# Optimization experiments

Hardware: AMD Instinct MI355X
Metric: run time of the kernel (lower is better)

Reference implementation:

```python
import jax, jax.numpy as jnp
import numpy as np

INPUT_DIM = 1024
OUTPUT_DIM = 1024


def setup_inputs() -> dict:
    key = jax.random.key(0)
    k1, k2, k3, k4 = jax.random.split(key, 4)
    B, S, D = 4, 2048, INPUT_DIM
    src = jax.random.normal(k1, (B, S, D), dtype=jnp.float32)
    tgt = jax.random.normal(k2, (B, S, D), dtype=jnp.float32)
    # nn.Linear(input_dim*2, output_dim): weight [out, in], bias [out]
    bound = 1.0 / np.sqrt(2 * D)
    W = jax.random.uniform(k3, (OUTPUT_DIM, 2 * D), jnp.float32, -bound, bound)
    b = jax.random.uniform(k4, (OUTPUT_DIM,), jnp.float32, -bound, bound)
    return {"src": src, "tgt": tgt, "W": W, "b": b}


def reference(src, tgt, W, b):
    # weight = bmm(tgt, src^T): [B, S_tgt, S_src]
    weight = jnp.einsum("btd,bsd->bts", tgt, src)
    # NOTE: original uses Softmax(dim=1) -> normalizes over the tgt axis
    weight = jax.nn.softmax(weight, axis=1)
    # weighted sum over src positions: [B, S_tgt, D]
    weight_sum = jnp.einsum("bts,bsd->btd", weight, src)
    output = jnp.concatenate([weight_sum, tgt], axis=2)  # [B, S_tgt, 2D]
    output = output @ W.T + b  # [B, S_tgt, output_dim]
    return (output, weight)
```

## Files before the change

kernel.cpp:

```cpp
#include <hip/hip_runtime.h>
#include <stdint.h>


#define B_   4
#define S_   2048
#define D_   1024
#define OUTD 1024

typedef unsigned short ushort_t;
typedef _Float16 half8 __attribute__((ext_vector_type(8)));
typedef float    f32x4 __attribute__((ext_vector_type(4)));

__device__ __forceinline__ ushort_t f2h(float f) {
    union { _Float16 h; ushort_t u; } v;
    v.h = (_Float16)f;
    return v.u;
}
__device__ __forceinline__ float h2f(ushort_t u) {
    union { _Float16 h; ushort_t u; } v;
    v.u = u;
    return (float)v.h;
}

__device__ __forceinline__ void ld16(const ushort_t* g, ushort_t* l) {
    __builtin_amdgcn_global_load_lds(
        (const __attribute__((address_space(1))) void*)g,
        (__attribute__((address_space(3))) void*)l, 16, 0, 0);
}


__global__ void k_split(const float4* __restrict__ src, const float4* __restrict__ tgt,
                        ushort4* __restrict__ sh,
                        ushort4* __restrict__ th, ushort4* __restrict__ tl)
{
    const int64_t n4 = (int64_t)B_ * S_ * D_ / 4;
    for (int64_t i = (int64_t)blockIdx.x * blockDim.x + threadIdx.x; i < n4;
         i += (int64_t)gridDim.x * blockDim.x) {
        float4 s = src[i];
        sh[i] = (ushort4){f2h(s.x), f2h(s.y), f2h(s.z), f2h(s.w)};
        float4 tv = tgt[i];
        ushort4 ht = {f2h(tv.x), f2h(tv.y), f2h(tv.z), f2h(tv.w)};
        th[i] = ht;
        tl[i] = (ushort4){f2h(tv.x - h2f(ht.x)), f2h(tv.y - h2f(ht.y)),
                          f2h(tv.z - h2f(ht.z)), f2h(tv.w - h2f(ht.w))};
    }
}

__global__ void k_wconv(const float4* __restrict__ W, ushort4* __restrict__ wb)
{
    const int64_t n4 = (int64_t)OUTD * 2 * D_ / 4;
    for (int64_t i = (int64_t)blockIdx.x * blockDim.x + threadIdx.x; i < n4;
         i += (int64_t)gridDim.x * blockDim.x) {
        float4 w = W[i];
        wb[i] = (ushort4){f2h(w.x), f2h(w.y), f2h(w.z), f2h(w.w)};
    }
}

__launch_bounds__(512, 2)
__global__ void k_gemm_logits(const ushort_t* __restrict__ Ah, const ushort_t* __restrict__ Al,
                              const ushort_t* __restrict__ Bs,
                              float* __restrict__ C,
                              float* __restrict__ pm, float* __restrict__ ps)
{
    const int M = S_, N = S_, K = D_;
    int b = blockIdx.z;
    Ah += (int64_t)b * M * K;  Al += (int64_t)b * M * K;
    Bs += (int64_t)b * N * K;
    C  += (int64_t)b * M * N;

    __shared__ __align__(16) ushort_t lds[2 * 24576];
    __shared__ float red_m[4][256], red_s[4][256];

    int t    = threadIdx.x;
    int m0   = blockIdx.y * 256, n0 = blockIdx.x * 256;
    int wave = t >> 6, lane = t & 63;
    int wr   = (wave >> 1) * 64;
    int wc   = (wave & 1) * 128;
    int l15  = lane & 15, quad = lane >> 4;

    f32x4 acc[4][8];
#pragma unroll
    for (int i = 0; i < 4; i++)
#pragma unroll
        for (int j = 0; j < 8; j++) acc[i][j] = (f32x4){0.f, 0.f, 0.f, 0.f};

    int pr   = t >> 3;
    int slot = t & 7;
    int cg   = slot ^ (pr & 7);
    int srow = pr * 2 + (cg >> 2);
    int scol = (cg & 3) * 8;

    const ushort_t* gAh = Ah + (int64_t)(m0 + srow) * K + scol;
    const ushort_t* gAl = Al + (int64_t)(m0 + srow) * K + scol;
    const ushort_t* gB  = Bs + (int64_t)(n0 + srow) * K + scol;
    const int64_t rstep = (int64_t)128 * K;

    auto stage = [&](int bufi, int kofs) {
        ushort_t* Lb = lds + bufi * 24576 + t * 8;
        ld16(gAh + kofs,         Lb);
        ld16(gAh + rstep + kofs, Lb + 4096);
        ld16(gAl + kofs,         Lb + 8192);
        ld16(gAl + rstep + kofs, Lb + 12288);
        ld16(gB  + kofs,         Lb + 16384);
        ld16(gB  + rstep + kofs, Lb + 20480);
    };

    int aoff[4], boff[8];
#pragma unroll
    for (int i = 0; i < 4; i++) {
        int R = wr + i * 16 + l15;
        int p = R >> 1, c = ((R & 1) << 2) + quad;
        aoff[i] = p * 64 + ((c ^ (p & 7)) << 3);
    }
#pragma unroll
    for (int j = 0; j < 8; j++) {
        int R = wc + j * 16 + l15;
        int p = R >> 1, c = ((R & 1) << 2) + quad;
        boff[j] = p * 64 + ((c ^ (p & 7)) << 3);
    }

    stage(0, 0);
    int buf = 0;

    for (int kt = 0; kt < 32; ++kt) {
        asm volatile("s_waitcnt vmcnt(0)" ::: "memory");
        __builtin_amdgcn_s_barrier();
        asm volatile("" ::: "memory");
        __builtin_amdgcn_sched_barrier(0);

        if (kt < 31) stage(buf ^ 1, (kt + 1) * 32);

        const ushort_t* Lb = lds + buf * 24576;
        half8 ah[4], al[4], bf[4];
#pragma unroll
        for (int i = 0; i < 4; i++) {
            ah[i] = *(const half8*)(Lb + aoff[i]);
            al[i] = *(const half8*)(Lb + 8192 + aoff[i]);
        }
#pragma unroll
        for (int j = 0; j < 4; j++) bf[j] = *(const half8*)(Lb + 16384 + boff[j]);

        __builtin_amdgcn_s_setprio(1);
#pragma unroll
        for (int i = 0; i < 4; i++)
#pragma unroll
            for (int j = 0; j < 4; j++)
                acc[i][j] = __builtin_amdgcn_mfma_f32_16x16x32_f16(ah[i], bf[j], acc[i][j], 0, 0, 0);
#pragma unroll
        for (int i = 0; i < 4; i++)
#pragma unroll
            for (int j = 0; j < 4; j++)
                acc[i][j] = __builtin_amdgcn_mfma_f32_16x16x32_f16(al[i], bf[j], acc[i][j], 0, 0, 0);
        __builtin_amdgcn_s_setprio(0);

#pragma unroll
        for (int j = 0; j < 4; j++) bf[j] = *(const half8*)(Lb + 16384 + boff[4 + j]);

        __builtin_amdgcn_s_setprio(1);
#pragma unroll
        for (int i = 0; i < 4; i++)
#pragma unroll
            for (int j = 0; j < 4; j++)
                acc[i][4 + j] = __builtin_amdgcn_mfma_f32_16x16x32_f16(ah[i], bf[j], acc[i][4 + j], 0, 0, 0);
#pragma unroll
        for (int i = 0; i < 4; i++)
#pragma unroll
            for (int j = 0; j < 4; j++)
                acc[i][4 + j] = __builtin_amdgcn_mfma_f32_16x16x32_f16(al[i], bf[j], acc[i][4 + j], 0, 0, 0);
        __builtin_amdgcn_s_setprio(0);

        buf ^= 1;
    }

#pragma unroll
    for (int i = 0; i < 4; i++) {
        int row_base = m0 + wr + i * 16 + quad * 4;
#pragma unroll
        for (int j = 0; j < 8; j++) {
            int col = n0 + wc + j * 16 + l15;
#pragma unroll
            for (int r = 0; r < 4; r++)
                C[(int64_t)(row_base + r) * N + col] = acc[i][j][r];
        }
    }

    int wrow = wave >> 1;
#pragma unroll
    for (int j = 0; j < 8; j++) {
        float m = -3.0e38f;
#pragma unroll
        for (int i = 0; i < 4; i++)
#pragma unroll
            for (int r = 0; r < 4; r++) m = fmaxf(m, acc[i][j][r]);
        float s = 0.f;
#pragma unroll
        for (int i = 0; i < 4; i++)
#pragma unroll
            for (int r = 0; r < 4; r++) s += __expf(acc[i][j][r] - m);
#pragma unroll
        for (int d = 16; d <= 32; d <<= 1) {
            float m2 = __shfl_xor(m, d, 64);
            float s2 = __shfl_xor(s, d, 64);
            float nm = fmaxf(m, m2);
            s = s * __expf(m - nm) + s2 * __expf(m2 - nm);
            m = nm;
        }
        if (lane < 16) {
            red_m[wrow][wc + j * 16 + l15] = m;
            red_s[wrow][wc + j * 16 + l15] = s;
        }
    }
    __syncthreads();
    if (t < 256) {
        float m = red_m[0][t];
#pragma unroll
        for (int w = 1; w < 4; w++) m = fmaxf(m, red_m[w][t]);
        float s = 0.f;
#pragma unroll
        for (int w = 0; w < 4; w++) s += red_s[w][t] * __expf(red_m[w][t] - m);
        int idx = blockIdx.y * (B_ * S_) + b * S_ + n0 + t;
        pm[idx] = m;
        ps[idx] = s;
    }
}


__global__ void k_colstats2(const float* __restrict__ pm, const float* __restrict__ ps,
                            float* __restrict__ cmax, float* __restrict__ cinv)
{
    int i = blockIdx.x * 256 + threadIdx.x;
    float m = -3.0e38f;
#pragma unroll
    for (int c = 0; c < 8; c++) m = fmaxf(m, pm[c * (B_ * S_) + i]);
    float sum = 0.f;
#pragma unroll
    for (int c = 0; c < 8; c++) sum += ps[c * (B_ * S_) + i] * __expf(pm[c * (B_ * S_) + i] - m);
    cmax[i] = m;
    cinv[i] = 1.0f / sum;
}

__global__ void k_softmax_norm(float4* __restrict__ L, const float4* __restrict__ cmax4,
                               const float4* __restrict__ cinv4, ushort4* __restrict__ wbf)
{
    const int64_t n4 = (int64_t)B_ * S_ * S_ / 4;
    for (int64_t i = (int64_t)blockIdx.x * blockDim.x + threadIdx.x; i < n4;
         i += (int64_t)gridDim.x * blockDim.x) {
        int b  = (int)(i >> 20);
        int c4 = (int)(i & 511);
        float4 x  = L[i];
        float4 cm = cmax4[b * 512 + c4];
        float4 ci = cinv4[b * 512 + c4];
        float4 w;
        w.x = __expf(x.x - cm.x) * ci.x;
        w.y = __expf(x.y - cm.y) * ci.y;
        w.z = __expf(x.z - cm.z) * ci.z;
        w.w = __expf(x.w - cm.w) * ci.w;
        L[i] = w;
        wbf[i] = (ushort4){f2h(w.x), f2h(w.y), f2h(w.z), f2h(w.w)};
    }
}

__launch_bounds__(256)
__global__ void k_gemm_nt_f16(const ushort_t* __restrict__ A, int lda, int64_t bsA,
                              const ushort_t* __restrict__ Bm, int ldb, int64_t bsB,
                              ushort_t* __restrict__ C, int ldc, int64_t bsC, int K)
{
    int b = blockIdx.z;
    A  += (int64_t)b * bsA;
    Bm += (int64_t)b * bsB;
    C  += (int64_t)b * bsC;

    __shared__ __align__(16) ushort_t sA[128 * 64], sB[128 * 64];

    int t    = threadIdx.x;
    int m0   = blockIdx.y * 128, n0 = blockIdx.x * 128;
    int wave = t >> 6, lane = t & 63;
    int wr   = (wave >> 1) * 64, wc = (wave & 1) * 64;
    int l15  = lane & 15, quad = lane >> 4;
    int e7   = l15 & 7;

    f32x4 acc[4][4];
#pragma unroll
    for (int i = 0; i < 4; i++)
#pragma unroll
        for (int j = 0; j < 4; j++) acc[i][j] = (f32x4){0.f, 0.f, 0.f, 0.f};

    int srow = t >> 3;
    int scol = (((t & 7) ^ (srow & 7)) * 8);

    const ushort_t* gA = A  + (int64_t)(m0 + srow) * lda + scol;
    const ushort_t* gB = Bm + (int64_t)(n0 + srow) * ldb + scol;
    ushort_t* lA = sA + wave * 512;
    ushort_t* lB = sB + wave * 512;

    for (int k0 = 0; k0 < K; k0 += 64) {
#pragma unroll
        for (int j = 0; j < 4; j++) {
            ld16(gA + (int64_t)(j * 32) * lda + k0, lA + j * 2048);
            ld16(gB + (int64_t)(j * 32) * ldb + k0, lB + j * 2048);
        }
        __syncthreads();
#pragma unroll
        for (int ks = 0; ks < 64; ks += 32) {
            int gchunk = (ks >> 3) + quad;
            int slot   = (gchunk ^ e7) * 8;
            half8 af[4], bf[4];
#pragma unroll
            for (int i = 0; i < 4; i++)
                af[i] = *(const half8*)(&sA[(wr + i * 16 + l15) * 64 + slot]);
#pragma unroll
            for (int j = 0; j < 4; j++)
                bf[j] = *(const half8*)(&sB[(wc + j * 16 + l15) * 64 + slot]);
#pragma unroll
            for (int i = 0; i < 4; i++)
#pragma unroll
                for (int j = 0; j < 4; j++)
                    acc[i][j] = __builtin_amdgcn_mfma_f32_16x16x32_f16(af[i], bf[j], acc[i][j], 0, 0, 0);
        }
        __syncthreads();
    }

#pragma unroll
    for (int i = 0; i < 4; i++) {
        int row_base = m0 + wr + i * 16 + quad * 4;
#pragma unroll
        for (int j = 0; j < 4; j++) {
            int col = n0 + wc + j * 16 + l15;
#pragma unroll
            for (int r = 0; r < 4; r++)
                C[(int64_t)(row_base + r) * ldc + col] = f2h(acc[i][j][r]);
        }
    }
}

__launch_bounds__(256)
__global__ void k_gemm_final(const ushort_t* __restrict__ Wt, const ushort_t* __restrict__ PT,
                             const ushort_t* __restrict__ Q, const float* __restrict__ bias,
                             float* __restrict__ out)
{
    const int K = S_, N = OUTD;
    int b = blockIdx.z;
    const ushort_t* A  = Wt + (int64_t)b * S_ * S_;
    const ushort_t* Bm = PT + (int64_t)b * OUTD * S_;
    const ushort_t* Qb = Q  + (int64_t)b * S_ * OUTD;
    float* Cb = out + (int64_t)b * S_ * OUTD;

    __shared__ __align__(16) ushort_t sA[128 * 64], sB[128 * 64];

    int t    = threadIdx.x;
    int m0   = blockIdx.y * 128, n0 = blockIdx.x * 128;
    int wave = t >> 6, lane = t & 63;
    int wr   = (wave >> 1) * 64, wc = (wave & 1) * 64;
    int l15  = lane & 15, quad = lane >> 4;
    int e7   = l15 & 7;

    f32x4 acc[4][4];
#pragma unroll
    for (int i = 0; i < 4; i++)
#pragma unroll
        for (int j = 0; j < 4; j++) acc[i][j] = (f32x4){0.f, 0.f, 0.f, 0.f};

    int srow = t >> 3;
    int scol = (((t & 7) ^ (srow & 7)) * 8);

    const ushort_t* gA = A  + (int64_t)(m0 + srow) * K + scol;
    const ushort_t* gB = Bm + (int64_t)(n0 + srow) * K + scol;
    ushort_t* lA = sA + wave * 512;
    ushort_t* lB = sB + wave * 512;

    for (int k0 = 0; k0 < K; k0 += 64) {
#pragma unroll
        for (int j = 0; j < 4; j++) {
            ld16(gA + (int64_t)(j * 32) * K + k0, lA + j * 2048);
            ld16(gB + (int64_t)(j * 32) * K + k0, lB + j * 2048);
        }
        __syncthreads();
#pragma unroll
        for (int ks = 0; ks < 64; ks += 32) {
            int gchunk = (ks >> 3) + quad;
            int slot   = (gchunk ^ e7) * 8;
            half8 af[4], bf[4];
#pragma unroll
            for (int i = 0; i < 4; i++)
                af[i] = *(const half8*)(&sA[(wr + i * 16 + l15) * 64 + slot]);
#pragma unroll
            for (int j = 0; j < 4; j++)
                bf[j] = *(const half8*)(&sB[(wc + j * 16 + l15) * 64 + slot]);
#pragma unroll
            for (int i = 0; i < 4; i++)
#pragma unroll
                for (int j = 0; j < 4; j++)
                    acc[i][j] = __builtin_amdgcn_mfma_f32_16x16x32_f16(af[i], bf[j], acc[i][j], 0, 0, 0);
        }
        __syncthreads();
    }

#pragma unroll
    for (int i = 0; i < 4; i++) {
        int row_base = m0 + wr + i * 16 + quad * 4;
#pragma unroll
        for (int j = 0; j < 4; j++) {
            int col = n0 + wc + j * 16 + l15;
            float bv = bias[col];
#pragma unroll
            for (int r = 0; r < 4; r++) {
                int64_t idx = (int64_t)(row_base + r) * N + col;
                Cb[idx] = acc[i][j][r] + h2f(Qb[idx]) + bv;
            }
        }
    }
}


extern "C" void kernel_launch(void* const* d_in, const int* in_sizes, int n_in,
                              void* d_out, int out_size, void* d_ws, size_t ws_size,
                              hipStream_t stream)
{
    const float* src  = (const float*)d_in[0];
    const float* tgt  = (const float*)d_in[1];
    const float* W    = (const float*)d_in[2];
    const float* bias = (const float*)d_in[3];

    float* out = (float*)d_out;
    float* Lw  = out + (size_t)B_ * S_ * OUTD;

    char*  ws = (char*)d_ws;
    size_t o  = 0;
    auto take = [&](size_t bytes) -> char* {
        char* p = ws + o;
        o += (bytes + 255) & ~(size_t)255;
        return p;
    };
    const size_t ELEMS = (size_t)B_ * S_ * D_;
    ushort_t* sh   = (ushort_t*)take(ELEMS * 2);
    ushort_t* th   = (ushort_t*)take(ELEMS * 2);
    ushort_t* tl   = (ushort_t*)take(ELEMS * 2);
    ushort_t* wbf  = (ushort_t*)take((size_t)B_ * S_ * S_ * 2);
    ushort_t* wb   = (ushort_t*)take((size_t)OUTD * 2 * D_ * 2);
    ushort_t* PT   = (ushort_t*)take((size_t)B_ * OUTD * S_ * 2);
    ushort_t* Qb   = (ushort_t*)take((size_t)B_ * S_ * OUTD * 2);
    float*    pm   = (float*)take(16 * (size_t)B_ * S_ * 4);
    float*    ps   = (float*)take(16 * (size_t)B_ * S_ * 4);
    float*    cmax = (float*)take((size_t)B_ * S_ * 4);
    float*    cinv = (float*)take((size_t)B_ * S_ * 4);
    (void)ws_size; (void)in_sizes; (void)n_in; (void)out_size;

    k_split<<<dim3(2048), dim3(256), 0, stream>>>((const float4*)src, (const float4*)tgt,
                                                  (ushort4*)sh, (ushort4*)th, (ushort4*)tl);
    k_wconv<<<dim3(512), dim3(256), 0, stream>>>((const float4*)W, (ushort4*)wb);

    k_gemm_nt_f16<<<dim3(16, 8, 4), dim3(256), 0, stream>>>(
        wb, 2 * D_, 0,
        sh, D_, (int64_t)S_ * D_,
        PT, S_, (int64_t)OUTD * S_, D_);

    k_gemm_nt_f16<<<dim3(8, 16, 4), dim3(256), 0, stream>>>(
        th, D_, (int64_t)S_ * D_,
        wb + D_, 2 * D_, 0,
        Qb, OUTD, (int64_t)S_ * OUTD, D_);

    k_gemm_logits<<<dim3(8, 8, 4), dim3(512), 0, stream>>>(th, tl, sh, Lw, pm, ps);

    k_colstats2<<<dim3(32), dim3(256), 0, stream>>>(pm, ps, cmax, cinv);
    k_softmax_norm<<<dim3(2048), dim3(256), 0, stream>>>((float4*)Lw, (const float4*)cmax,
                                                         (const float4*)cinv, (ushort4*)wbf);

    k_gemm_final<<<dim3(8, 16, 4), dim3(256), 0, stream>>>(wbf, PT, Qb, bias, out);
}
```

Baseline: 358.5 us.

## Double-buffer LDS and enlarge tiles to 256x128 in fp16 GEMM kernels

```diff
diff --git a/kernel.cpp b/kernel.cpp
--- a/kernel.cpp
+++ b/kernel.cpp
@@ -260,24 +260,24 @@
     }
 }
 
-__launch_bounds__(256)
-__global__ void k_gemm_nt_f16(const ushort_t* __restrict__ A, int lda, int64_t bsA,
-                              const ushort_t* __restrict__ Bm, int ldb, int64_t bsB,
-                              ushort_t* __restrict__ C, int ldc, int64_t bsC, int K)
+__launch_bounds__(512, 2)
+__global__ void k_gemm_nt2(const ushort_t* __restrict__ A, int lda, int64_t bsA,
+                           const ushort_t* __restrict__ Bm, int ldb, int64_t bsB,
+                           ushort_t* __restrict__ C, int ldc, int64_t bsC, int K)
 {
     int b = blockIdx.z;
     A  += (int64_t)b * bsA;
     Bm += (int64_t)b * bsB;
     C  += (int64_t)b * bsC;
 
-    __shared__ __align__(16) ushort_t sA[128 * 64], sB[128 * 64];
+    __shared__ __align__(16) ushort_t lds[2 * 24576];
 
     int t    = threadIdx.x;
-    int m0   = blockIdx.y * 128, n0 = blockIdx.x * 128;
+    int m0   = blockIdx.y * 256, n0 = blockIdx.x * 128;
     int wave = t >> 6, lane = t & 63;
-    int wr   = (wave >> 1) * 64, wc = (wave & 1) * 64;
+    int wr   = (wave >> 1) * 64;
+    int wc   = (wave & 1) * 64;
     int l15  = lane & 15, quad = lane >> 4;
-    int e7   = l15 & 7;
 
     f32x4 acc[4][4];
 #pragma unroll
@@ -286,38 +286,71 @@
         for (int j = 0; j < 4; j++) acc[i][j] = (f32x4){0.f, 0.f, 0.f, 0.f};
 
     int srow = t >> 3;
-    int scol = (((t & 7) ^ (srow & 7)) * 8);
+    int cg   = (t & 7) ^ (srow & 7);
+    int scol = cg * 8;
 
     const ushort_t* gA = A  + (int64_t)(m0 + srow) * lda + scol;
     const ushort_t* gB = Bm + (int64_t)(n0 + srow) * ldb + scol;
-    ushort_t* lA = sA + wave * 512;
-    ushort_t* lB = sB + wave * 512;
-
-    for (int k0 = 0; k0 < K; k0 += 64) {
-#pragma unroll
-        for (int j = 0; j < 4; j++) {
-            ld16(gA + (int64_t)(j * 32) * lda + k0, lA + j * 2048);
-            ld16(gB + (int64_t)(j * 32) * ldb + k0, lB + j * 2048);
-        }
-        __syncthreads();
-#pragma unroll
-        for (int ks = 0; ks < 64; ks += 32) {
-            int gchunk = (ks >> 3) + quad;
-            int slot   = (gchunk ^ e7) * 8;
+
+    auto stage = [&](int bufi, int k0) {
+        ushort_t* Lb = lds + bufi * 24576 + t * 8;
+        ld16(gA + k0,                        Lb);
+        ld16(gA + (int64_t)64  * lda + k0,   Lb + 4096);
+        ld16(gA + (int64_t)128 * lda + k0,   Lb + 8192);
+        ld16(gA + (int64_t)192 * lda + k0,   Lb + 12288);
+        ld16(gB + k0,                        Lb + 16384);
+        ld16(gB + (int64_t)64  * ldb + k0,   Lb + 20480);
+    };
+
+    int aoff[4][2], boff[4][2];
+#pragma unroll
+    for (int i = 0; i < 4; i++) {
+        int R = wr + i * 16 + l15;
+#pragma unroll
+        for (int h = 0; h < 2; h++) {
+            int c = quad + h * 4;
+            aoff[i][h] = R * 64 + ((c ^ (R & 7)) << 3);
+        }
+    }
+#pragma unroll
+    for (int j = 0; j < 4; j++) {
+        int R = wc + j * 16 + l15;
+#pragma unroll
+        for (int h = 0; h < 2; h++) {
+            int c = quad + h * 4;
+            boff[j][h] = 16384 + R * 64 + ((c ^ (R & 7)) << 3);
+        }
+    }
+
+    stage(0, 0);
+    int buf = 0;
+    const int NT = K >> 6;
+
+    for (int kt = 0; kt < NT; ++kt) {
+        asm volatile("s_waitcnt vmcnt(0)" ::: "memory");
+        __builtin_amdgcn_s_barrier();
+        asm volatile("" ::: "memory");
+        __builtin_amdgcn_sched_barrier(0);
+
+        if (kt + 1 < NT) stage(buf ^ 1, (kt + 1) * 64);
+
+        const ushort_t* Lb = lds + buf * 24576;
+#pragma unroll
+        for (int h = 0; h < 2; h++) {
             half8 af[4], bf[4];
 #pragma unroll
-            for (int i = 0; i < 4; i++)
-                af[i] = *(const half8*)(&sA[(wr + i * 16 + l15) * 64 + slot]);
-#pragma unroll
-            for (int j = 0; j < 4; j++)
-                bf[j] = *(const half8*)(&sB[(wc + j * 16 + l15) * 64 + slot]);
+            for (int i = 0; i < 4; i++) af[i] = *(const half8*)(Lb + aoff[i][h]);
+#pragma unroll
+            for (int j = 0; j < 4; j++) bf[j] = *(const half8*)(Lb + boff[j][h]);
+            __builtin_amdgcn_s_setprio(1);
 #pragma unroll
             for (int i = 0; i < 4; i++)
 #pragma unroll
                 for (int j = 0; j < 4; j++)
                     acc[i][j] = __builtin_amdgcn_mfma_f32_16x16x32_f16(af[i], bf[j], acc[i][j], 0, 0, 0);
-        }
-        __syncthreads();
+            __builtin_amdgcn_s_setprio(0);
+        }
+        buf ^= 1;
     }
 
 #pragma unroll
@@ -333,7 +366,7 @@
     }
 }
 
-__launch_bounds__(256)
+__launch_bounds__(512, 2)
 __global__ void k_gemm_final(const ushort_t* __restrict__ Wt, const ushort_t* __restrict__ PT,
                              const ushort_t* __restrict__ Q, const float* __restrict__ bias,
                              float* __restrict__ out)
@@ -345,14 +378,14 @@
     const ushort_t* Qb = Q  + (int64_t)b * S_ * OUTD;
     float* Cb = out + (int64_t)b * S_ * OUTD;
 
-    __shared__ __align__(16) ushort_t sA[128 * 64], sB[128 * 64];
+    __shared__ __align__(16) ushort_t lds[2 * 24576];
 
     int t    = threadIdx.x;
-    int m0   = blockIdx.y * 128, n0 = blockIdx.x * 128;
+    int m0   = blockIdx.y * 256, n0 = blockIdx.x * 128;
     int wave = t >> 6, lane = t & 63;
-    int wr   = (wave >> 1) * 64, wc = (wave & 1) * 64;
+    int wr   = (wave >> 1) * 64;
+    int wc   = (wave & 1) * 64;
     int l15  = lane & 15, quad = lane >> 4;
-    int e7   = l15 & 7;
 
     f32x4 acc[4][4];
 #pragma unroll
@@ -361,38 +394,71 @@
         for (int j = 0; j < 4; j++) acc[i][j] = (f32x4){0.f, 0.f, 0.f, 0.f};
 
     int srow = t >> 3;
-    int scol = (((t & 7) ^ (srow & 7)) * 8);
+    int cg   = (t & 7) ^ (srow & 7);
+    int scol = cg * 8;
 
     const ushort_t* gA = A  + (int64_t)(m0 + srow) * K + scol;
     const ushort_t* gB = Bm + (int64_t)(n0 + srow) * K + scol;
-    ushort_t* lA = sA + wave * 512;
-    ushort_t* lB = sB + wave * 512;
-
-    for (int k0 = 0; k0 < K; k0 += 64) {
-#pragma unroll
-        for (int j = 0; j < 4; j++) {
-            ld16(gA + (int64_t)(j * 32) * K + k0, lA + j * 2048);
-            ld16(gB + (int64_t)(j * 32) * K + k0, lB + j * 2048);
-        }
-        __syncthreads();
-#pragma unroll
-        for (int ks = 0; ks < 64; ks += 32) {
-            int gchunk = (ks >> 3) + quad;
-            int slot   = (gchunk ^ e7) * 8;
+
+    auto stage = [&](int bufi, int k0) {
+        ushort_t* Lb = lds + bufi * 24576 + t * 8;
+        ld16(gA + k0,                      Lb);
+        ld16(gA + (int64_t)64  * K + k0,   Lb + 4096);
+        ld16(gA + (int64_t)128 * K + k0,   Lb + 8192);
+        ld16(gA + (int64_t)192 * K + k0,   Lb + 12288);
+        ld16(gB + k0,                      Lb + 16384);
+        ld16(gB + (int64_t)64  * K + k0,   Lb + 20480);
+    };
+
+    int aoff[4][2], boff[4][2];
+#pragma unroll
+    for (int i = 0; i < 4; i++) {
+        int R = wr + i * 16 + l15;
+#pragma unroll
+        for (int h = 0; h < 2; h++) {
+            int c = quad + h * 4;
+            aoff[i][h] = R * 64 + ((c ^ (R & 7)) << 3);
+        }
+    }
+#pragma unroll
+    for (int j = 0; j < 4; j++) {
+        int R = wc + j * 16 + l15;
+#pragma unroll
+        for (int h = 0; h < 2; h++) {
+            int c = quad + h * 4;
+            boff[j][h] = 16384 + R * 64 + ((c ^ (R & 7)) << 3);
+        }
+    }
+
+    stage(0, 0);
+    int buf = 0;
+    const int NT = K >> 6;
+
+    for (int kt = 0; kt < NT; ++kt) {
+        asm volatile("s_waitcnt vmcnt(0)" ::: "memory");
+        __builtin_amdgcn_s_barrier();
+        asm volatile("" ::: "memory");
+        __builtin_amdgcn_sched_barrier(0);
+
+        if (kt + 1 < NT) stage(buf ^ 1, (kt + 1) * 64);
+
+        const ushort_t* Lb = lds + buf * 24576;
+#pragma unroll
+        for (int h = 0; h < 2; h++) {
             half8 af[4], bf[4];
 #pragma unroll
-            for (int i = 0; i < 4; i++)
-                af[i] = *(const half8*)(&sA[(wr + i * 16 + l15) * 64 + slot]);
-#pragma unroll
-            for (int j = 0; j < 4; j++)
-                bf[j] = *(const half8*)(&sB[(wc + j * 16 + l15) * 64 + slot]);
+            for (int i = 0; i < 4; i++) af[i] = *(const half8*)(Lb + aoff[i][h]);
+#pragma unroll
+            for (int j = 0; j < 4; j++) bf[j] = *(const half8*)(Lb + boff[j][h]);
+            __builtin_amdgcn_s_setprio(1);
 #pragma unroll
             for (int i = 0; i < 4; i++)
 #pragma unroll
                 for (int j = 0; j < 4; j++)
                     acc[i][j] = __builtin_amdgcn_mfma_f32_16x16x32_f16(af[i], bf[j], acc[i][j], 0, 0, 0);
-        }
-        __syncthreads();
+            __builtin_amdgcn_s_setprio(0);
+        }
+        buf ^= 1;
     }
 
 #pragma unroll
@@ -449,12 +515,12 @@
                                                   (ushort4*)sh, (ushort4*)th, (ushort4*)tl);
     k_wconv<<<dim3(512), dim3(256), 0, stream>>>((const float4*)W, (ushort4*)wb);
 
-    k_gemm_nt_f16<<<dim3(16, 8, 4), dim3(256), 0, stream>>>(
+    k_gemm_nt2<<<dim3(16, 4, 4), dim3(512), 0, stream>>>(
         wb, 2 * D_, 0,
         sh, D_, (int64_t)S_ * D_,
         PT, S_, (int64_t)OUTD * S_, D_);
 
-    k_gemm_nt_f16<<<dim3(8, 16, 4), dim3(256), 0, stream>>>(
+    k_gemm_nt2<<<dim3(8, 8, 4), dim3(512), 0, stream>>>(
         th, D_, (int64_t)S_ * D_,
         wb + D_, 2 * D_, 0,
         Qb, OUTD, (int64_t)S_ * OUTD, D_);
@@ -465,5 +531,5 @@
     k_softmax_norm<<<dim3(2048), dim3(256), 0, stream>>>((float4*)Lw, (const float4*)cmax,
                                                          (const float4*)cinv, (ushort4*)wbf);
 
-    k_gemm_final<<<dim3(8, 16, 4), dim3(256), 0, stream>>>(wbf, PT, Qb, bias, out);
-}
+    k_gemm_final<<<dim3(8, 8, 4), dim3(512), 0, stream>>>(wbf, PT, Qb, bias, out);
+}
```

Result: faster. 347.7 us (-3.0%).
